# Kernel optimization log

Measured on AMD Instinct MI355X. Metric: run time of the kernel, lower is better.

The kernel has to match this reference:

```python
import jax, jax.numpy as jnp
import numpy as np

DEG = 2
KNOTS = (0.25, 0.5, 0.75)
CONDITION_DIM = 1
INPUT_DIM = 1024
OUTPUT_DIM = 1024
NUM_BASIS = DEG + 1 + len(KNOTS)  # 6
BATCH = 32768


def setup_inputs() -> dict:
    key = jax.random.key(0)
    k1, k2, k3 = jax.random.split(key, 3)
    # x carries [features | condition] concatenated along dim 1
    x = jax.random.uniform(k1, (BATCH, INPUT_DIM + CONDITION_DIM), dtype=jnp.float32)
    fan_in = INPUT_DIM  # kaiming-style scale for the weight tensor
    weight = jax.random.normal(k2, (NUM_BASIS * CONDITION_DIM, INPUT_DIM, OUTPUT_DIM), dtype=jnp.float32) / np.sqrt(fan_in)
    bias_param = jax.random.normal(k3, (OUTPUT_DIM,), dtype=jnp.float32) / np.sqrt(fan_in)
    return {"x": x, "weight": weight, "bias_param": bias_param}


def _basis(condition):
    # condition: (B, condition_dim). Truncated power spline basis per condition column.
    cols = []
    for j in range(CONDITION_DIM):
        t = condition[:, j]
        for i in range(DEG + 1):
            cols.append(t ** i)
        for knot in KNOTS:
            cols.append(jax.nn.relu(t - knot) ** DEG)
    return jnp.stack(cols, axis=1)  # (B, coef_dim)


def reference(x, weight, bias_param):
    feats = x[:, :INPUT_DIM]            # (B, d)
    condition = x[:, INPUT_DIM:]        # (B, condition_dim)
    basis = _basis(condition)           # (B, c)
    # Same math as einsum('bc,cde->bde') then ('bde,bd->be'), but contracted in
    # the cheaper order (avoids the (B, d, e) per-sample weight tensor):
    xw = jnp.einsum('bd,cde->bce', feats, weight)   # (B, c, e)
    out = jnp.einsum('bc,bce->be', basis, xw)       # (B, e)
    return out + bias_param
```

## Files before the change

### kernel.cpp

```cpp
#include <hip/hip_runtime.h>
#include <stdint.h>

#define IN_DIM    1024
#define OUT_DIM   1024
#define ROWSTRIDE 1025
#define BATCH     32768
#define NBASIS    6
#define KTOT      (NBASIS * IN_DIM)
#define KSTEPS    (KTOT / 64)

typedef __bf16 bf16x8 __attribute__((ext_vector_type(8)));
typedef float  f32x4  __attribute__((ext_vector_type(4)));

__device__ inline unsigned short f2bf(float f) {
  union { float f; unsigned u; } v; v.f = f;
  unsigned u = v.u;
  return (unsigned short)((u + 0x7FFFu + ((u >> 16) & 1u)) >> 16);
}

__global__ void prep_feats(const float* __restrict__ x, unsigned short* __restrict__ A2) {
  const int b = blockIdx.x;
  const int tid = threadIdx.x;
  const float* xr = x + (size_t)b * ROWSTRIDE;
  const float t = xr[IN_DIM];
  float bas[NBASIS];
  bas[0] = 1.0f; bas[1] = t; bas[2] = t * t;
  float r1 = fmaxf(t - 0.25f, 0.0f);
  float r2 = fmaxf(t - 0.50f, 0.0f);
  float r3 = fmaxf(t - 0.75f, 0.0f);
  bas[3] = r1 * r1; bas[4] = r2 * r2; bas[5] = r3 * r3;

  unsigned short* arow = A2 + (size_t)b * KTOT;
  #pragma unroll
  for (int k = 0; k < 2; ++k) {
    int d = k * 512 + tid * 2;
    float v0 = xr[d], v1 = xr[d + 1];
    #pragma unroll
    for (int c = 0; c < NBASIS; ++c) {
      union { unsigned short u[2]; unsigned int w; } p;
      p.u[0] = f2bf(bas[c] * v0);
      p.u[1] = f2bf(bas[c] * v1);
      *(unsigned int*)(arow + c * IN_DIM + d) = p.w;
    }
  }
}

__global__ void prep_wt(const float* __restrict__ w, unsigned short* __restrict__ bt) {
  __shared__ unsigned short t[32][33];
  int k0 = blockIdx.x * 32;
  int e0 = blockIdx.y * 32;
  int tid = threadIdx.x;
  #pragma unroll
  for (int p = tid; p < 1024; p += 256) {
    int kk = p >> 5, ee = p & 31;
    t[ee][kk] = f2bf(w[(size_t)(k0 + kk) * OUT_DIM + e0 + ee]);
  }
  __syncthreads();
  #pragma unroll
  for (int p = tid; p < 1024; p += 256) {
    int ee = p >> 5, kk = p & 31;
    bt[(size_t)(e0 + ee) * KTOT + k0 + kk] = t[ee][kk];
  }
}

__device__ inline void gload_lds16(const unsigned short* g, unsigned short* l) {
  __builtin_amdgcn_global_load_lds((const __attribute__((address_space(1))) void*)g,
                                   (__attribute__((address_space(3))) void*)l, 16, 0, 0);
}

__global__ __launch_bounds__(256, 3) void vcl_gemm(
    const unsigned short* __restrict__ A2,
    const unsigned short* __restrict__ BT,
    const float* __restrict__ bias,
    float* __restrict__ out) {
  __shared__ unsigned short smem[2 * 128 * 64];
  unsigned short* sA = smem;
  unsigned short* sB = smem + 128 * 64;

  const int tid = threadIdx.x;
  const int bm0 = (blockIdx.x >> 3) * 128;
  const int bn0 = (blockIdx.x & 7) * 128;

  const int wv   = tid >> 6;
  const int lane = tid & 63;
  const int lr   = lane >> 3;
  const int kc   = (lane & 7) ^ lr;
  const int ln15 = lane & 15;
  const int quad = lane >> 4;
  const int wm   = wv >> 1, wn = wv & 1;
  const int cs0  = quad ^ (ln15 & 7);
  const int cs1  = (4 + quad) ^ (ln15 & 7);

  const unsigned short* gA[4];
  const unsigned short* gB[4];
  unsigned short* lA[4];
  unsigned short* lB[4];
  #pragma unroll
  for (int wc = 0; wc < 4; ++wc) {
    int r = wv * 32 + wc * 8 + lr;
    gA[wc] = A2 + (size_t)(bm0 + r) * KTOT + kc * 8;
    gB[wc] = BT + (size_t)(bn0 + r) * KTOT + kc * 8;
    lA[wc] = sA + (wv * 4 + wc) * 512;
    lB[wc] = sB + (wv * 4 + wc) * 512;
  }

  float bias_j[4];
  #pragma unroll
  for (int j = 0; j < 4; ++j)
    bias_j[j] = bias[bn0 + wn * 64 + j * 16 + ln15];

  f32x4 acc[4][4] = {};

  #pragma unroll
  for (int wc = 0; wc < 4; ++wc) {
    gload_lds16(gA[wc], lA[wc]);
    gload_lds16(gB[wc], lB[wc]);
  }

  for (int t = 0; t < KSTEPS; ++t) {
    __syncthreads();

    bf16x8 bfr2[2][4];
    #pragma unroll
    for (int j = 0; j < 4; ++j) {
      int nt = wn * 64 + j * 16 + ln15;
      bfr2[0][j] = *(const bf16x8*)(sB + nt * 64 + cs0 * 8);
      bfr2[1][j] = *(const bf16x8*)(sB + nt * 64 + cs1 * 8);
    }
    #pragma unroll
    for (int i = 0; i < 4; ++i) {
      int rowt = wm * 64 + i * 16 + ln15;
      bf16x8 af0 = *(const bf16x8*)(sA + rowt * 64 + cs0 * 8);
      bf16x8 af1 = *(const bf16x8*)(sA + rowt * 64 + cs1 * 8);
      #pragma unroll
      for (int j = 0; j < 4; ++j) {
        acc[i][j] = __builtin_amdgcn_mfma_f32_16x16x32_bf16(af0, bfr2[0][j], acc[i][j], 0, 0, 0);
        acc[i][j] = __builtin_amdgcn_mfma_f32_16x16x32_bf16(af1, bfr2[1][j], acc[i][j], 0, 0, 0);
      }
    }

    __syncthreads();
    if (t + 1 < KSTEPS) {
      const int kOff = (t + 1) * 64;
      #pragma unroll
      for (int wc = 0; wc < 4; ++wc) {
        gload_lds16(gA[wc] + kOff, lA[wc]);
        gload_lds16(gB[wc] + kOff, lB[wc]);
      }
    }
  }

  float* buf = (float*)smem;
  const int ROWP = 132;
  const int erow = tid >> 3;
  const int echk = tid & 7;
  const int grow_base = bm0 + (erow >> 4) * 64 + (erow & 15);
  const int gcol = bn0 + echk * 16;

  #pragma unroll
  for (int i = 0; i < 4; ++i) {
    __syncthreads();
    #pragma unroll
    for (int j = 0; j < 4; ++j) {
      int cr = wm * 16 + quad * 4;
      int cc = wn * 64 + j * 16 + ln15;
      #pragma unroll
      for (int r = 0; r < 4; ++r)
        buf[(cr + r) * ROWP + cc] = acc[i][j][r] + bias_j[j];
    }
    __syncthreads();
    float* orow = out + (size_t)(grow_base + i * 16) * OUT_DIM + gcol;
    const float* brow = buf + erow * ROWP + echk * 16;
    #pragma unroll
    for (int e = 0; e < 4; ++e)
      *(f32x4*)(orow + e * 4) = *(const f32x4*)(brow + e * 4);
  }
}

extern "C" void kernel_launch(void* const* d_in, const int* in_sizes, int n_in,
                              void* d_out, int out_size, void* d_ws, size_t ws_size,
                              hipStream_t stream) {
  const float* x    = (const float*)d_in[0];
  const float* w    = (const float*)d_in[1];
  const float* bias = (const float*)d_in[2];
  float* out = (float*)d_out;

  unsigned short* A2 = (unsigned short*)d_ws;
  unsigned short* BT = (unsigned short*)((char*)d_ws + (size_t)BATCH * KTOT * 2);

  prep_feats<<<BATCH, 256, 0, stream>>>(x, A2);
  dim3 g2(KTOT / 32, OUT_DIM / 32);
  prep_wt<<<g2, 256, 0, stream>>>(w, BT);
  vcl_gemm<<<(BATCH / 128) * (OUT_DIM / 128), 256, 0, stream>>>(A2, BT, bias, out);
}
```

Measured before the change: 772.1 us.

## Apply spline basis in epilogue per basis chunk instead of materializing scaled features

Features are no longer pre-multiplied by the six basis values into a 6x-wide bf16 A matrix. Only bf16 features are stored, plus a transposed basis table. The GEMM reuses the same A tile for each basis chunk of K and folds acc into a second accumulator scaled by the per-row basis value every 16 k-steps. This removes most of the A-side memory traffic and the large prep write, at the cost of doubled accumulator registers (launch bounds lowered to 2 waves/SIMD) and extra FMA work at chunk boundaries.

```diff
diff --git a/kernel.cpp b/kernel.cpp
--- a/kernel.cpp
+++ b/kernel.cpp
@@ -7,7 +7,7 @@
 #define BATCH     32768
 #define NBASIS    6
 #define KTOT      (NBASIS * IN_DIM)
-#define KSTEPS    (KTOT / 64)
+#define KSTEPS    96
 
 typedef __bf16 bf16x8 __attribute__((ext_vector_type(8)));
 typedef float  f32x4  __attribute__((ext_vector_type(4)));
@@ -18,30 +18,35 @@
   return (unsigned short)((u + 0x7FFFu + ((u >> 16) & 1u)) >> 16);
 }
 
-__global__ void prep_feats(const float* __restrict__ x, unsigned short* __restrict__ A2) {
+__global__ void prep_f(const float* __restrict__ x,
+                       unsigned short* __restrict__ F,
+                       float* __restrict__ bas_t) {
   const int b = blockIdx.x;
   const int tid = threadIdx.x;
   const float* xr = x + (size_t)b * ROWSTRIDE;
-  const float t = xr[IN_DIM];
-  float bas[NBASIS];
-  bas[0] = 1.0f; bas[1] = t; bas[2] = t * t;
-  float r1 = fmaxf(t - 0.25f, 0.0f);
-  float r2 = fmaxf(t - 0.50f, 0.0f);
-  float r3 = fmaxf(t - 0.75f, 0.0f);
-  bas[3] = r1 * r1; bas[4] = r2 * r2; bas[5] = r3 * r3;
-
-  unsigned short* arow = A2 + (size_t)b * KTOT;
+  unsigned short* frow = F + (size_t)b * IN_DIM;
+
   #pragma unroll
   for (int k = 0; k < 2; ++k) {
     int d = k * 512 + tid * 2;
-    float v0 = xr[d], v1 = xr[d + 1];
-    #pragma unroll
-    for (int c = 0; c < NBASIS; ++c) {
-      union { unsigned short u[2]; unsigned int w; } p;
-      p.u[0] = f2bf(bas[c] * v0);
-      p.u[1] = f2bf(bas[c] * v1);
-      *(unsigned int*)(arow + c * IN_DIM + d) = p.w;
-    }
+    union { unsigned short u[2]; unsigned int w; } p;
+    p.u[0] = f2bf(xr[d]);
+    p.u[1] = f2bf(xr[d + 1]);
+    *(unsigned int*)(frow + d) = p.w;
+  }
+
+  if (tid < 6) {
+    float t  = xr[IN_DIM];
+    float r1 = fmaxf(t - 0.25f, 0.0f);
+    float r2 = fmaxf(t - 0.50f, 0.0f);
+    float r3 = fmaxf(t - 0.75f, 0.0f);
+    float v = (tid == 0) ? 1.0f
+            : (tid == 1) ? t
+            : (tid == 2) ? t * t
+            : (tid == 3) ? r1 * r1
+            : (tid == 4) ? r2 * r2
+            :              r3 * r3;
+    bas_t[(size_t)tid * BATCH + b] = v;
   }
 }
 
@@ -68,12 +73,14 @@
                                    (__attribute__((address_space(3))) void*)l, 16, 0, 0);
 }
 
-__global__ __launch_bounds__(256, 3) void vcl_gemm(
-    const unsigned short* __restrict__ A2,
+__global__ __launch_bounds__(256, 2) void vcl_gemm(
+    const unsigned short* __restrict__ F,
     const unsigned short* __restrict__ BT,
+    const float* __restrict__ bas_t,
     const float* __restrict__ bias,
     float* __restrict__ out) {
   __shared__ unsigned short smem[2 * 128 * 64];
+  __shared__ __align__(16) float bas_lds[NBASIS * 128];
   unsigned short* sA = smem;
   unsigned short* sB = smem + 128 * 64;
 
@@ -91,6 +98,9 @@
   const int cs0  = quad ^ (ln15 & 7);
   const int cs1  = (4 + quad) ^ (ln15 & 7);
 
+  for (int p = tid; p < NBASIS * 128; p += 256)
+    bas_lds[p] = bas_t[(size_t)(p >> 7) * BATCH + bm0 + (p & 127)];
+
   const unsigned short* gA[4];
   const unsigned short* gB[4];
   unsigned short* lA[4];
@@ -98,8 +108,8 @@
   #pragma unroll
   for (int wc = 0; wc < 4; ++wc) {
     int r = wv * 32 + wc * 8 + lr;
-    gA[wc] = A2 + (size_t)(bm0 + r) * KTOT + kc * 8;
-    gB[wc] = BT + (size_t)(bn0 + r) * KTOT + kc * 8;
+    gA[wc] = F  + (size_t)(bm0 + r) * IN_DIM + kc * 8;
+    gB[wc] = BT + (size_t)(bn0 + r) * KTOT   + kc * 8;
     lA[wc] = sA + (wv * 4 + wc) * 512;
     lB[wc] = sB + (wv * 4 + wc) * 512;
   }
@@ -109,7 +119,8 @@
   for (int j = 0; j < 4; ++j)
     bias_j[j] = bias[bn0 + wn * 64 + j * 16 + ln15];
 
-  f32x4 acc[4][4] = {};
+  f32x4 acc[4][4]  = {};
+  f32x4 accO[4][4] = {};
 
   #pragma unroll
   for (int wc = 0; wc < 4; ++wc) {
@@ -141,11 +152,27 @@
 
     __syncthreads();
     if (t + 1 < KSTEPS) {
-      const int kOff = (t + 1) * 64;
+      const int offA = ((t + 1) & 15) * 64;
+      const int offB = (t + 1) * 64;
       #pragma unroll
       for (int wc = 0; wc < 4; ++wc) {
-        gload_lds16(gA[wc] + kOff, lA[wc]);
-        gload_lds16(gB[wc] + kOff, lB[wc]);
+        gload_lds16(gA[wc] + offA, lA[wc]);
+        gload_lds16(gB[wc] + offB, lB[wc]);
+      }
+    }
+
+    if ((t & 15) == 15) {
+      const int c = t >> 4;
+      #pragma unroll
+      for (int i = 0; i < 4; ++i) {
+        f32x4 bb = *(const f32x4*)(&bas_lds[c * 128 + wm * 64 + i * 16 + quad * 4]);
+        #pragma unroll
+        for (int j = 0; j < 4; ++j) {
+          #pragma unroll
+          for (int r = 0; r < 4; ++r)
+            accO[i][j][r] += bb[r] * acc[i][j][r];
+          acc[i][j] = (f32x4){0.0f, 0.0f, 0.0f, 0.0f};
+        }
       }
     }
   }
@@ -166,7 +193,7 @@
       int cc = wn * 64 + j * 16 + ln15;
       #pragma unroll
       for (int r = 0; r < 4; ++r)
-        buf[(cr + r) * ROWP + cc] = acc[i][j][r] + bias_j[j];
+        buf[(cr + r) * ROWP + cc] = accO[i][j][r] + bias_j[j];
     }
     __syncthreads();
     float* orow = out + (size_t)(grow_base + i * 16) * OUT_DIM + gcol;
@@ -185,11 +212,12 @@
   const float* bias = (const float*)d_in[2];
   float* out = (float*)d_out;
 
-  unsigned short* A2 = (unsigned short*)d_ws;
-  unsigned short* BT = (unsigned short*)((char*)d_ws + (size_t)BATCH * KTOT * 2);
-
-  prep_feats<<<BATCH, 256, 0, stream>>>(x, A2);
+  unsigned short* F  = (unsigned short*)d_ws;
+  unsigned short* BT = (unsigned short*)((char*)d_ws + (size_t)BATCH * IN_DIM * 2);
+  float* bas_t = (float*)((char*)d_ws + (size_t)BATCH * IN_DIM * 2 + (size_t)OUT_DIM * KTOT * 2);
+
+  prep_f<<<BATCH, 256, 0, stream>>>(x, F, bas_t);
   dim3 g2(KTOT / 32, OUT_DIM / 32);
   prep_wt<<<g2, 256, 0, stream>>>(w, BT);
-  vcl_gemm<<<(BATCH / 128) * (OUT_DIM / 128), 256, 0, stream>>>(A2, BT, bias, out);
-}
+  vcl_gemm<<<(BATCH / 128) * (OUT_DIM / 128), 256, 0, stream>>>(F, BT, bas_t, bias, out);
+}
```

New measurement: 692.9 us. 10.3% less time.
